# Performance work log

Hardware: AMD Instinct MI355X
Metric: run time of the kernel (lower is better)

The kernel has to match this reference:

```python
import jax, jax.numpy as jnp
import numpy as np

C_IN = 128      # in_channels == num_hiddens (required for residual add)
C_RES = 64      # num_residual_hiddens
D = 512         # representation_dim (in == out)


def _complete_conv1d(x, W, Wc, bc):
    """Faithful fused form of CompleteConv1d.forward for batch=1.

    x:  (1, C, D)   input
    W:  (C, D, D)   stacked per-channel Linear weights (W[c] maps D->D)
    Wc: (OC, C)     1x1 Conv1d weight (kernel dim squeezed)
    bc: (OC,)       1x1 Conv1d bias

    The autograd jacobian of the per-channel linear map is block diagonal:
      xy_grad[c, o, c', i] = W[c, o, i] * delta(c, c')
    so xy_grad_reduced[o, i] = sum_c W[c, o, i], node[i] = argmax_o of that,
    and the python double loop is a scatter-add:
      (y - y_neg)[0, f, n] = sum_{i : node[i]==n} W[f, n, i] * x[0, f, i]
    (y itself, including the Linear biases, cancels exactly).
    """
    d = W.shape[1]
    node = jnp.argmax(jnp.sum(W, axis=0), axis=0)          # (D,) argmax over o
    idx = jnp.arange(d)
    vals = W[:, node, idx] * x[0]                           # (C, D): W[f,node[i],i]*x[0,f,i]
    diff = jnp.zeros_like(x[0]).at[:, node].add(vals)       # scatter-add over repeated nodes
    out = jnp.einsum('oc,cd->od', Wc, diff) + bc[:, None]   # 1x1 conv == channel GEMM
    return out[None]                                        # (1, OC, D)


def setup_inputs() -> dict:
    key = jax.random.key(0)
    ks = jax.random.split(key, 7)
    s = lambda k, shape, scale: (jax.random.normal(k, shape, dtype=jnp.float32) * scale)
    return {
        'x':   s(ks[0], (1, C_IN, D), 1.0),
        'W1':  s(ks[1], (C_IN, D, D), D ** -0.5),
        'Wc1': s(ks[2], (C_RES, C_IN), C_IN ** -0.5),
        'bc1': s(ks[3], (C_RES,), 0.02),
        'W2':  s(ks[4], (C_RES, D, D), D ** -0.5),
        'Wc2': s(ks[5], (C_IN, C_RES), C_RES ** -0.5),
        'bc2': s(ks[6], (C_IN,), 0.02),
    }


def reference(x, W1, Wc1, bc1, W2, Wc2, bc2):
    # nn.ReLU(True) inside the Sequential mutates x in place, so the residual
    # add uses relu(x), not x.
    xr = jax.nn.relu(x)
    h1 = _complete_conv1d(xr, W1, Wc1, bc1)
    h2 = _complete_conv1d(jax.nn.relu(h1), W2, Wc2, bc2)
    return xr + h2
```

## Files before the change

kernel.cpp:

```cpp
#include <hip/hip_runtime.h>

#define C_IN  128
#define C_RES 64
#define D     512
#define DD    (D * D)

template <int C>
__device__ inline float4 colsum(const float4* __restrict__ Wp) {
    float4 acc = make_float4(0.f, 0.f, 0.f, 0.f);
#pragma unroll 16
    for (int c = 0; c < C; ++c) {
        float4 w = Wp[(size_t)c * (DD / 4)];
        acc.x += w.x; acc.y += w.y; acc.z += w.z; acc.w += w.w;
    }
    return acc;
}

__global__ void sum_zero_kernel(const float* __restrict__ W1,
                                const float* __restrict__ W2,
                                float* __restrict__ S1,
                                float* __restrict__ S2,
                                float* __restrict__ diff_zero) {
    int t = blockIdx.x * 256 + threadIdx.x;
    if (t < DD / 4) {
        ((float4*)S1)[t] = colsum<C_IN>((const float4*)W1 + t);
    } else {
        int t2 = t - DD / 4;
        ((float4*)S2)[t2] = colsum<C_RES>((const float4*)W2 + t2);
    }
    diff_zero[t] = 0.f;
}

__global__ void argmax_scatter_kernel(const float* __restrict__ S1,
                                      const float* __restrict__ S2,
                                      const float* __restrict__ W1,
                                      const float* __restrict__ W2,
                                      const float* __restrict__ x,
                                      float* __restrict__ diff1,
                                      float* __restrict__ w2v,
                                      int* __restrict__ node2) {
    __shared__ float lv[256];
    __shared__ int   li[256];
    __shared__ int   node_s[16];

    const int  tid = threadIdx.x;
    const bool st1 = blockIdx.x < 32;
    const int  i0  = (blockIdx.x & 31) * 16;
    const float* __restrict__ S = st1 ? S1 : S2;

    const int il = tid & 15;
    const int ol = tid >> 4;
    float best = -__builtin_inff();
    int   bidx = D;
#pragma unroll 4
    for (int k = 0; k < 32; ++k) {
        int o = ol + (k << 4);
        float v = S[o * D + i0 + il];
        if (v > best) { best = v; bidx = o; }
    }
    lv[tid] = best; li[tid] = bidx;
    __syncthreads();
    for (int s = 128; s >= 16; s >>= 1) {
        if (tid < s) {
            float v2 = lv[tid + s]; int i2 = li[tid + s];
            if (v2 > lv[tid] || (v2 == lv[tid] && i2 < li[tid])) {
                lv[tid] = v2; li[tid] = i2;
            }
        }
        __syncthreads();
    }
    if (tid < 16) {
        node_s[tid] = li[tid];
        if (!st1) node2[i0 + tid] = li[tid];
    }
    __syncthreads();

    if (st1) {
        for (int idx = tid; idx < C_IN * 16; idx += 256) {
            int ii = idx & 15;
            int c  = idx >> 4;
            int i  = i0 + ii;
            int n  = node_s[ii];
            float xv = fmaxf(x[c * D + i], 0.f);
            float w  = W1[(size_t)c * DD + (size_t)n * D + i];
            atomicAdd(&diff1[c * D + n], w * xv);
        }
    } else {
        for (int idx = tid; idx < C_RES * 16; idx += 256) {
            int ii = idx & 15;
            int c  = idx >> 4;
            int i  = i0 + ii;
            int n  = node_s[ii];
            w2v[c * D + i] = W2[(size_t)c * DD + (size_t)n * D + i];
        }
    }
}

__global__ void conv1_scatter2_kernel(const float* __restrict__ Wc1,
                                      const float* __restrict__ bc1,
                                      const float* __restrict__ diff1,
                                      const float* __restrict__ w2v,
                                      const int* __restrict__ node2,
                                      float* __restrict__ diff2) {
    __shared__ float wc[C_IN];
    const int c = blockIdx.x >> 1;
    const int i = ((blockIdx.x & 1) << 8) + threadIdx.x;
    if (threadIdx.x < C_IN) wc[threadIdx.x] = Wc1[c * C_IN + threadIdx.x];
    __syncthreads();

    float acc = bc1[c];
#pragma unroll 8
    for (int cc = 0; cc < C_IN; ++cc)
        acc += wc[cc] * diff1[cc * D + i];
    float x2 = fmaxf(acc, 0.f);
    int n = node2[i];
    atomicAdd(&diff2[c * D + n], w2v[c * D + i] * x2);
}

__global__ void final_kernel(const float* __restrict__ Wc2,
                             const float* __restrict__ bc2,
                             const float* __restrict__ diff2,
                             const float* __restrict__ x,
                             float* __restrict__ out) {
    __shared__ float wc[C_RES];
    const int o = blockIdx.x >> 1;
    const int d = ((blockIdx.x & 1) << 8) + threadIdx.x;
    if (threadIdx.x < C_RES) wc[threadIdx.x] = Wc2[o * C_RES + threadIdx.x];
    __syncthreads();

    float acc = bc2[o];
#pragma unroll 8
    for (int c = 0; c < C_RES; ++c)
        acc += wc[c] * diff2[c * D + d];
    out[o * D + d] = acc + fmaxf(x[o * D + d], 0.f);
}

extern "C" void kernel_launch(void* const* d_in, const int* in_sizes, int n_in,
                              void* d_out, int out_size, void* d_ws, size_t ws_size,
                              hipStream_t stream) {
    const float* x   = (const float*)d_in[0];
    const float* W1  = (const float*)d_in[1];
    const float* Wc1 = (const float*)d_in[2];
    const float* bc1 = (const float*)d_in[3];
    const float* W2  = (const float*)d_in[4];
    const float* Wc2 = (const float*)d_in[5];
    const float* bc2 = (const float*)d_in[6];
    float* out = (float*)d_out;

    float* ws    = (float*)d_ws;
    float* S1    = ws;
    float* S2    = S1 + DD;
    float* diff1 = S2 + DD;
    float* diff2 = diff1 + C_IN * D;
    float* w2v   = diff2 + C_RES * D;
    int*   node2 = (int*)(w2v + C_RES * D);

    sum_zero_kernel<<<384, 256, 0, stream>>>(W1, W2, S1, S2, diff1);
    argmax_scatter_kernel<<<64, 256, 0, stream>>>(S1, S2, W1, W2, x,
                                                  diff1, w2v, node2);
    conv1_scatter2_kernel<<<128, 256, 0, stream>>>(Wc1, bc1, diff1, w2v,
                                                   node2, diff2);
    final_kernel<<<256, 256, 0, stream>>>(Wc2, bc2, diff2, x, out);
}
```

Baseline: 256.5 us.

## Fuse all stages into one cooperative kernel with grid syncs and rebalanced colsum

Replaces the four separate kernel launches with a single cooperative kernel that separates its stages with grid.sync(). The W1 column sum is split into two 64-channel halves, so each of the 384 blocks does equal work (two 64-channel sums per thread) instead of some blocks summing 128 channels and others 64. The argmax/scatter stage now uses 128 blocks of 8 columns instead of 64 blocks of 16. This is meant to cut launch overhead and the load-imbalance tail, at the cost of grid-wide barriers and an extra partial-sum buffer that the argmax stage must read.

New measurement: 407.6 us. 58.9% more time.

```diff
diff --git a/kernel.cpp b/kernel.cpp
--- a/kernel.cpp
+++ b/kernel.cpp
@@ -1,138 +1,150 @@
 #include <hip/hip_runtime.h>
+#include <hip/hip_cooperative_groups.h>
+
+namespace cg = cooperative_groups;
 
 #define C_IN  128
 #define C_RES 64
 #define D     512
 #define DD    (D * D)
+#define NC4   (DD / 4)
 
-template <int C>
-__device__ inline float4 colsum(const float4* __restrict__ Wp) {
+__device__ __forceinline__ float4 colsum64(const float4* __restrict__ p) {
     float4 acc = make_float4(0.f, 0.f, 0.f, 0.f);
 #pragma unroll 16
-    for (int c = 0; c < C; ++c) {
-        float4 w = Wp[(size_t)c * (DD / 4)];
+    for (int c = 0; c < 64; ++c) {
+        float4 w = p[(size_t)c * NC4];
         acc.x += w.x; acc.y += w.y; acc.z += w.z; acc.w += w.w;
     }
     return acc;
 }
 
-__global__ void sum_zero_kernel(const float* __restrict__ W1,
-                                const float* __restrict__ W2,
-                                float* __restrict__ S1,
-                                float* __restrict__ S2,
-                                float* __restrict__ diff_zero) {
-    int t = blockIdx.x * 256 + threadIdx.x;
-    if (t < DD / 4) {
-        ((float4*)S1)[t] = colsum<C_IN>((const float4*)W1 + t);
-    } else {
-        int t2 = t - DD / 4;
-        ((float4*)S2)[t2] = colsum<C_RES>((const float4*)W2 + t2);
-    }
-    diff_zero[t] = 0.f;
-}
+__global__ void fused_kernel(const float* __restrict__ x,
+                             const float* __restrict__ W1,
+                             const float* __restrict__ Wc1,
+                             const float* __restrict__ bc1,
+                             const float* __restrict__ W2,
+                             const float* __restrict__ Wc2,
+                             const float* __restrict__ bc2,
+                             float* __restrict__ out,
+                             float* __restrict__ ws) {
+    cg::grid_group grid = cg::this_grid();
 
-__global__ void argmax_scatter_kernel(const float* __restrict__ S1,
-                                      const float* __restrict__ S2,
-                                      const float* __restrict__ W1,
-                                      const float* __restrict__ W2,
-                                      const float* __restrict__ x,
-                                      float* __restrict__ diff1,
-                                      float* __restrict__ w2v,
-                                      int* __restrict__ node2) {
+    float* S1lo  = ws;
+    float* S1hi  = S1lo + DD;
+    float* S2    = S1hi + DD;
+    float* diff1 = S2 + DD;
+    float* diff2 = diff1 + C_IN * D;
+    float* w2v   = diff2 + C_RES * D;
+    int*   node2 = (int*)(w2v + C_RES * D);
+
+    const int tid = threadIdx.x;
+    const int bid = blockIdx.x;
+    const int u   = bid * 256 + tid;
+
     __shared__ float lv[256];
     __shared__ int   li[256];
-    __shared__ int   node_s[16];
+    __shared__ int   node_s[8];
 
-    const int  tid = threadIdx.x;
-    const bool st1 = blockIdx.x < 32;
-    const int  i0  = (blockIdx.x & 31) * 16;
-    const float* __restrict__ S = st1 ? S1 : S2;
+    {
+        if (u < NC4) {
+            ((float4*)S1lo)[u] = colsum64((const float4*)W1 + u);
+        } else {
+            int t = u - NC4;
+            ((float4*)S1hi)[t] =
+                colsum64((const float4*)W1 + (size_t)64 * NC4 + t);
+        }
+        if (u < NC4 / 2) {
+            int t = u + NC4 / 2;
+            ((float4*)S1hi)[t] =
+                colsum64((const float4*)W1 + (size_t)64 * NC4 + t);
+        } else {
+            int t = u - NC4 / 2;
+            ((float4*)S2)[t] = colsum64((const float4*)W2 + t);
+        }
+        diff1[u] = 0.f;
+    }
+    grid.sync();
 
-    const int il = tid & 15;
-    const int ol = tid >> 4;
-    float best = -__builtin_inff();
-    int   bidx = D;
-#pragma unroll 4
-    for (int k = 0; k < 32; ++k) {
-        int o = ol + (k << 4);
-        float v = S[o * D + i0 + il];
-        if (v > best) { best = v; bidx = o; }
-    }
-    lv[tid] = best; li[tid] = bidx;
-    __syncthreads();
-    for (int s = 128; s >= 16; s >>= 1) {
-        if (tid < s) {
-            float v2 = lv[tid + s]; int i2 = li[tid + s];
-            if (v2 > lv[tid] || (v2 == lv[tid] && i2 < li[tid])) {
-                lv[tid] = v2; li[tid] = i2;
+    if (bid < 128) {
+        const bool st1 = bid < 64;
+        const int  i0  = (bid & 63) * 8;
+        const int  il  = tid & 7;
+        const int  ol  = tid >> 3;
+        float best = -__builtin_inff();
+        int   bidx = D;
+#pragma unroll
+        for (int k = 0; k < 16; ++k) {
+            int o = ol + (k << 5);
+            float v = st1 ? (S1lo[o * D + i0 + il] + S1hi[o * D + i0 + il])
+                          : S2[o * D + i0 + il];
+            if (v > best) { best = v; bidx = o; }
+        }
+        lv[tid] = best; li[tid] = bidx;
+        __syncthreads();
+        for (int s = 128; s >= 8; s >>= 1) {
+            if (tid < s) {
+                float v2 = lv[tid + s]; int i2 = li[tid + s];
+                if (v2 > lv[tid] || (v2 == lv[tid] && i2 < li[tid])) {
+                    lv[tid] = v2; li[tid] = i2;
+                }
+            }
+            __syncthreads();
+        }
+        if (tid < 8) {
+            node_s[tid] = li[tid];
+            if (!st1) node2[i0 + tid] = li[tid];
+        }
+        __syncthreads();
+
+        if (st1) {
+            for (int idx = tid; idx < C_IN * 8; idx += 256) {
+                int ii = idx & 7;
+                int c  = idx >> 3;
+                int i  = i0 + ii;
+                int n  = node_s[ii];
+                float xv = fmaxf(x[c * D + i], 0.f);
+                float w  = W1[(size_t)c * DD + (size_t)n * D + i];
+                atomicAdd(&diff1[c * D + n], w * xv);
+            }
+        } else {
+            for (int idx = tid; idx < C_RES * 8; idx += 256) {
+                int ii = idx & 7;
+                int c  = idx >> 3;
+                int i  = i0 + ii;
+                int n  = node_s[ii];
+                w2v[c * D + i] = W2[(size_t)c * DD + (size_t)n * D + i];
             }
         }
+    }
+    grid.sync();
+
+    if (bid < 128) {
+        const int c = bid >> 1;
+        const int i = ((bid & 1) << 8) + tid;
+        if (tid < C_IN) lv[tid] = Wc1[c * C_IN + tid];
         __syncthreads();
+        float acc = bc1[c];
+#pragma unroll 8
+        for (int cc = 0; cc < C_IN; ++cc)
+            acc += lv[cc] * diff1[cc * D + i];
+        float x2 = fmaxf(acc, 0.f);
+        int n = node2[i];
+        atomicAdd(&diff2[c * D + n], w2v[c * D + i] * x2);
     }
-    if (tid < 16) {
-        node_s[tid] = li[tid];
-        if (!st1) node2[i0 + tid] = li[tid];
+    grid.sync();
+
+    if (bid < 256) {
+        const int o = bid >> 1;
+        const int d = ((bid & 1) << 8) + tid;
+        if (tid < C_RES) lv[tid] = Wc2[o * C_RES + tid];
+        __syncthreads();
+        float acc = bc2[o];
+#pragma unroll 8
+        for (int c = 0; c < C_RES; ++c)
+            acc += lv[c] * diff2[c * D + d];
+        out[o * D + d] = acc + fmaxf(x[o * D + d], 0.f);
     }
-    __syncthreads();
-
-    if (st1) {
-        for (int idx = tid; idx < C_IN * 16; idx += 256) {
-            int ii = idx & 15;
-            int c  = idx >> 4;
-            int i  = i0 + ii;
-            int n  = node_s[ii];
-            float xv = fmaxf(x[c * D + i], 0.f);
-            float w  = W1[(size_t)c * DD + (size_t)n * D + i];
-            atomicAdd(&diff1[c * D + n], w * xv);
-        }
-    } else {
-        for (int idx = tid; idx < C_RES * 16; idx += 256) {
-            int ii = idx & 15;
-            int c  = idx >> 4;
-            int i  = i0 + ii;
-            int n  = node_s[ii];
-            w2v[c * D + i] = W2[(size_t)c * DD + (size_t)n * D + i];
-        }
-    }
-}
-
-__global__ void conv1_scatter2_kernel(const float* __restrict__ Wc1,
-                                      const float* __restrict__ bc1,
-                                      const float* __restrict__ diff1,
-                                      const float* __restrict__ w2v,
-                                      const int* __restrict__ node2,
-                                      float* __restrict__ diff2) {
-    __shared__ float wc[C_IN];
-    const int c = blockIdx.x >> 1;
-    const int i = ((blockIdx.x & 1) << 8) + threadIdx.x;
-    if (threadIdx.x < C_IN) wc[threadIdx.x] = Wc1[c * C_IN + threadIdx.x];
-    __syncthreads();
-
-    float acc = bc1[c];
-#pragma unroll 8
-    for (int cc = 0; cc < C_IN; ++cc)
-        acc += wc[cc] * diff1[cc * D + i];
-    float x2 = fmaxf(acc, 0.f);
-    int n = node2[i];
-    atomicAdd(&diff2[c * D + n], w2v[c * D + i] * x2);
-}
-
-__global__ void final_kernel(const float* __restrict__ Wc2,
-                             const float* __restrict__ bc2,
-                             const float* __restrict__ diff2,
-                             const float* __restrict__ x,
-                             float* __restrict__ out) {
-    __shared__ float wc[C_RES];
-    const int o = blockIdx.x >> 1;
-    const int d = ((blockIdx.x & 1) << 8) + threadIdx.x;
-    if (threadIdx.x < C_RES) wc[threadIdx.x] = Wc2[o * C_RES + threadIdx.x];
-    __syncthreads();
-
-    float acc = bc2[o];
-#pragma unroll 8
-    for (int c = 0; c < C_RES; ++c)
-        acc += wc[c] * diff2[c * D + d];
-    out[o * D + d] = acc + fmaxf(x[o * D + d], 0.f);
 }
 
 extern "C" void kernel_launch(void* const* d_in, const int* in_sizes, int n_in,
@@ -146,19 +158,10 @@
     const float* Wc2 = (const float*)d_in[5];
     const float* bc2 = (const float*)d_in[6];
     float* out = (float*)d_out;
+    float* ws  = (float*)d_ws;
 
-    float* ws    = (float*)d_ws;
-    float* S1    = ws;
-    float* S2    = S1 + DD;
-    float* diff1 = S2 + DD;
-    float* diff2 = diff1 + C_IN * D;
-    float* w2v   = diff2 + C_RES * D;
-    int*   node2 = (int*)(w2v + C_RES * D);
-
-    sum_zero_kernel<<<384, 256, 0, stream>>>(W1, W2, S1, S2, diff1);
-    argmax_scatter_kernel<<<64, 256, 0, stream>>>(S1, S2, W1, W2, x,
-                                                  diff1, w2v, node2);
-    conv1_scatter2_kernel<<<128, 256, 0, stream>>>(Wc1, bc1, diff1, w2v,
-                                                   node2, diff2);
-    final_kernel<<<256, 256, 0, stream>>>(Wc2, bc2, diff2, x, out);
+    void* args[] = {(void*)&x, (void*)&W1, (void*)&Wc1, (void*)&bc1,
+                    (void*)&W2, (void*)&Wc2, (void*)&bc2, (void*)&out, (void*)&ws};
+    hipLaunchCooperativeKernel((const void*)fused_kernel, dim3(384), dim3(256),
+                               args, 0, stream);
 }
```

## Split channel column-sum into partial planes and widen argmax grid

Applied to the files above, without the earlier changes.

The channel reduction of W1 and W2 is split into six 32-channel partial-sum planes, so the first kernel launches 1536 blocks instead of 384 and gives the memory-bound pass over roughly 200 MB of weights more parallelism. The argmax kernel finishes the reduction by adding four or two partial planes per element. It now handles 4 columns per block across 256 blocks instead of 16 columns across 64. This costs extra workspace and extra partial-sum traffic in exchange for better bandwidth use and occupancy.

Result: slower. 267.9 us (+4.4%).

```diff
diff --git a/kernel.cpp b/kernel.cpp
--- a/kernel.cpp
+++ b/kernel.cpp
@@ -4,35 +4,29 @@
 #define C_RES 64
 #define D     512
 #define DD    (D * D)
-
-template <int C>
-__device__ inline float4 colsum(const float4* __restrict__ Wp) {
-    float4 acc = make_float4(0.f, 0.f, 0.f, 0.f);
-#pragma unroll 16
-    for (int c = 0; c < C; ++c) {
-        float4 w = Wp[(size_t)c * (DD / 4)];
-        acc.x += w.x; acc.y += w.y; acc.z += w.z; acc.w += w.w;
-    }
-    return acc;
-}
+#define NC4   (DD / 4)
 
 __global__ void sum_zero_kernel(const float* __restrict__ W1,
                                 const float* __restrict__ W2,
-                                float* __restrict__ S1,
-                                float* __restrict__ S2,
+                                float* __restrict__ Sp,
                                 float* __restrict__ diff_zero) {
     int t = blockIdx.x * 256 + threadIdx.x;
-    if (t < DD / 4) {
-        ((float4*)S1)[t] = colsum<C_IN>((const float4*)W1 + t);
-    } else {
-        int t2 = t - DD / 4;
-        ((float4*)S2)[t2] = colsum<C_RES>((const float4*)W2 + t2);
+    int plane = t >> 16;
+    int chunk = t & 0xFFFF;
+    const float4* p = (plane < 4)
+        ? (const float4*)W1 + (size_t)plane * 32 * NC4 + chunk
+        : (const float4*)W2 + (size_t)(plane - 4) * 32 * NC4 + chunk;
+    float4 acc = make_float4(0.f, 0.f, 0.f, 0.f);
+#pragma unroll 16
+    for (int c = 0; c < 32; ++c) {
+        float4 w = p[(size_t)c * NC4];
+        acc.x += w.x; acc.y += w.y; acc.z += w.z; acc.w += w.w;
     }
-    diff_zero[t] = 0.f;
+    ((float4*)Sp)[t] = acc;
+    if (t < (C_IN + C_RES) * D) diff_zero[t] = 0.f;
 }
 
-__global__ void argmax_scatter_kernel(const float* __restrict__ S1,
-                                      const float* __restrict__ S2,
+__global__ void argmax_scatter_kernel(const float* __restrict__ Sp,
                                       const float* __restrict__ W1,
                                       const float* __restrict__ W2,
                                       const float* __restrict__ x,
@@ -41,26 +35,32 @@
                                       int* __restrict__ node2) {
     __shared__ float lv[256];
     __shared__ int   li[256];
-    __shared__ int   node_s[16];
+    __shared__ int   node_s[4];
 
     const int  tid = threadIdx.x;
-    const bool st1 = blockIdx.x < 32;
-    const int  i0  = (blockIdx.x & 31) * 16;
-    const float* __restrict__ S = st1 ? S1 : S2;
+    const bool st1 = blockIdx.x < 128;
+    const int  i0  = (blockIdx.x & 127) * 4;
+    const int  il  = tid & 3;
+    const int  ol  = tid >> 2;
+    const float* __restrict__ S1p = Sp;
+    const float* __restrict__ S2p = Sp + (size_t)4 * DD;
 
-    const int il = tid & 15;
-    const int ol = tid >> 4;
     float best = -__builtin_inff();
     int   bidx = D;
-#pragma unroll 4
-    for (int k = 0; k < 32; ++k) {
-        int o = ol + (k << 4);
-        float v = S[o * D + i0 + il];
+#pragma unroll
+    for (int k = 0; k < 8; ++k) {
+        int o   = ol + (k << 6);
+        int off = o * D + i0 + il;
+        float v;
+        if (st1)
+            v = S1p[off] + S1p[DD + off] + S1p[2 * DD + off] + S1p[3 * DD + off];
+        else
+            v = S2p[off] + S2p[DD + off];
         if (v > best) { best = v; bidx = o; }
     }
     lv[tid] = best; li[tid] = bidx;
     __syncthreads();
-    for (int s = 128; s >= 16; s >>= 1) {
+    for (int s = 128; s >= 4; s >>= 1) {
         if (tid < s) {
             float v2 = lv[tid + s]; int i2 = li[tid + s];
             if (v2 > lv[tid] || (v2 == lv[tid] && i2 < li[tid])) {
@@ -69,16 +69,16 @@
         }
         __syncthreads();
     }
-    if (tid < 16) {
+    if (tid < 4) {
         node_s[tid] = li[tid];
         if (!st1) node2[i0 + tid] = li[tid];
     }
     __syncthreads();
 
     if (st1) {
-        for (int idx = tid; idx < C_IN * 16; idx += 256) {
-            int ii = idx & 15;
-            int c  = idx >> 4;
+        for (int idx = tid; idx < C_IN * 4; idx += 256) {
+            int ii = idx & 3;
+            int c  = idx >> 2;
             int i  = i0 + ii;
             int n  = node_s[ii];
             float xv = fmaxf(x[c * D + i], 0.f);
@@ -86,9 +86,9 @@
             atomicAdd(&diff1[c * D + n], w * xv);
         }
     } else {
-        for (int idx = tid; idx < C_RES * 16; idx += 256) {
-            int ii = idx & 15;
-            int c  = idx >> 4;
+        for (int idx = tid; idx < C_RES * 4; idx += 256) {
+            int ii = idx & 3;
+            int c  = idx >> 2;
             int i  = i0 + ii;
             int n  = node_s[ii];
             w2v[c * D + i] = W2[(size_t)c * DD + (size_t)n * D + i];
@@ -148,16 +148,15 @@
     float* out = (float*)d_out;
 
     float* ws    = (float*)d_ws;
-    float* S1    = ws;
-    float* S2    = S1 + DD;
-    float* diff1 = S2 + DD;
+    float* Sp    = ws;
+    float* diff1 = Sp + (size_t)6 * DD;
     float* diff2 = diff1 + C_IN * D;
     float* w2v   = diff2 + C_RES * D;
     int*   node2 = (int*)(w2v + C_RES * D);
 
-    sum_zero_kernel<<<384, 256, 0, stream>>>(W1, W2, S1, S2, diff1);
-    argmax_scatter_kernel<<<64, 256, 0, stream>>>(S1, S2, W1, W2, x,
-                                                  diff1, w2v, node2);
+    sum_zero_kernel<<<1536, 256, 0, stream>>>(W1, W2, Sp, diff1);
+    argmax_scatter_kernel<<<256, 256, 0, stream>>>(Sp, W1, W2, x,
+                                                   diff1, w2v, node2);
     conv1_scatter2_kernel<<<128, 256, 0, stream>>>(Wc1, bc1, diff1, w2v,
                                                    node2, diff2);
     final_kernel<<<256, 256, 0, stream>>>(Wc2, bc2, diff2, x, out);
```

## Balance column-sum work by splitting W1 sum and fuse tail conv stages

Applied to the files above, without the earlier changes.

The column-sum kernel now gives every thread two 64-channel column sums, with W1 split into low and high halves that the argmax kernel adds back together, so the W1 and W2 threads carry equal load. The output is initialized with relu(x)+bc2 during the first kernel. The two 1x1-conv kernels are merged into one tail kernel that computes h1 for 8 positions per block and then applies Wc2 before scattering, using linearity so the diff2 buffer and a launch go away. This trades extra atomics into out and a duplicated Wc1 load per block for removing the load imbalance and one kernel launch.

Measured after the change: 290.9 us. +13.4%, slower.

```diff
diff --git a/kernel.cpp b/kernel.cpp
--- a/kernel.cpp
+++ b/kernel.cpp
@@ -4,41 +4,58 @@
 #define C_RES 64
 #define D     512
 #define DD    (D * D)
+#define NC4   (DD / 4)
 
-template <int C>
-__device__ inline float4 colsum(const float4* __restrict__ Wp) {
+__device__ __forceinline__ float4 colsum64(const float4* __restrict__ p) {
     float4 acc = make_float4(0.f, 0.f, 0.f, 0.f);
 #pragma unroll 16
-    for (int c = 0; c < C; ++c) {
-        float4 w = Wp[(size_t)c * (DD / 4)];
+    for (int c = 0; c < 64; ++c) {
+        float4 w = p[(size_t)c * NC4];
         acc.x += w.x; acc.y += w.y; acc.z += w.z; acc.w += w.w;
     }
     return acc;
 }
 
-__global__ void sum_zero_kernel(const float* __restrict__ W1,
-                                const float* __restrict__ W2,
-                                float* __restrict__ S1,
-                                float* __restrict__ S2,
-                                float* __restrict__ diff_zero) {
-    int t = blockIdx.x * 256 + threadIdx.x;
-    if (t < DD / 4) {
-        ((float4*)S1)[t] = colsum<C_IN>((const float4*)W1 + t);
+__global__ __launch_bounds__(256)
+void sum_init_kernel(const float* __restrict__ W1,
+                     const float* __restrict__ W2,
+                     const float* __restrict__ x,
+                     const float* __restrict__ bc2,
+                     float* __restrict__ S1lo,
+                     float* __restrict__ S1hi,
+                     float* __restrict__ S2,
+                     float* __restrict__ diff1,
+                     float* __restrict__ out) {
+    const int u = blockIdx.x * 256 + threadIdx.x;
+    if (u < NC4) {
+        ((float4*)S1lo)[u] = colsum64((const float4*)W1 + u);
     } else {
-        int t2 = t - DD / 4;
-        ((float4*)S2)[t2] = colsum<C_RES>((const float4*)W2 + t2);
+        int t = u - NC4;
+        ((float4*)S1hi)[t] = colsum64((const float4*)W1 + (size_t)64 * NC4 + t);
     }
-    diff_zero[t] = 0.f;
+    if (u < NC4 / 2) {
+        int t = u + NC4 / 2;
+        ((float4*)S1hi)[t] = colsum64((const float4*)W1 + (size_t)64 * NC4 + t);
+    } else {
+        int t = u - NC4 / 2;
+        ((float4*)S2)[t] = colsum64((const float4*)W2 + t);
+    }
+    if (u < C_IN * D) {
+        diff1[u] = 0.f;
+        out[u] = fmaxf(x[u], 0.f) + bc2[u >> 9];
+    }
 }
 
-__global__ void argmax_scatter_kernel(const float* __restrict__ S1,
-                                      const float* __restrict__ S2,
-                                      const float* __restrict__ W1,
-                                      const float* __restrict__ W2,
-                                      const float* __restrict__ x,
-                                      float* __restrict__ diff1,
-                                      float* __restrict__ w2v,
-                                      int* __restrict__ node2) {
+__global__ __launch_bounds__(256)
+void argmax_scatter_kernel(const float* __restrict__ S1lo,
+                           const float* __restrict__ S1hi,
+                           const float* __restrict__ S2,
+                           const float* __restrict__ W1,
+                           const float* __restrict__ W2,
+                           const float* __restrict__ x,
+                           float* __restrict__ diff1,
+                           float* __restrict__ w2v,
+                           int* __restrict__ node2) {
     __shared__ float lv[256];
     __shared__ int   li[256];
     __shared__ int   node_s[16];
@@ -46,16 +63,16 @@
     const int  tid = threadIdx.x;
     const bool st1 = blockIdx.x < 32;
     const int  i0  = (blockIdx.x & 31) * 16;
-    const float* __restrict__ S = st1 ? S1 : S2;
+    const int  il  = tid & 15;
+    const int  ol  = tid >> 4;
 
-    const int il = tid & 15;
-    const int ol = tid >> 4;
     float best = -__builtin_inff();
     int   bidx = D;
 #pragma unroll 4
     for (int k = 0; k < 32; ++k) {
-        int o = ol + (k << 4);
-        float v = S[o * D + i0 + il];
+        int o   = ol + (k << 4);
+        int off = o * D + i0 + il;
+        float v = st1 ? (S1lo[off] + S1hi[off]) : S2[off];
         if (v > best) { best = v; bidx = o; }
     }
     lv[tid] = best; li[tid] = bidx;
@@ -96,43 +113,62 @@
     }
 }
 
-__global__ void conv1_scatter2_kernel(const float* __restrict__ Wc1,
-                                      const float* __restrict__ bc1,
-                                      const float* __restrict__ diff1,
-                                      const float* __restrict__ w2v,
-                                      const int* __restrict__ node2,
-                                      float* __restrict__ diff2) {
-    __shared__ float wc[C_IN];
-    const int c = blockIdx.x >> 1;
-    const int i = ((blockIdx.x & 1) << 8) + threadIdx.x;
-    if (threadIdx.x < C_IN) wc[threadIdx.x] = Wc1[c * C_IN + threadIdx.x];
+__global__ __launch_bounds__(256)
+void tail_kernel(const float* __restrict__ Wc1,
+                 const float* __restrict__ bc1,
+                 const float* __restrict__ diff1,
+                 const float* __restrict__ w2v,
+                 const int* __restrict__ node2,
+                 const float* __restrict__ Wc2,
+                 float* __restrict__ out) {
+    __shared__ float wc1s[C_RES][C_IN + 1];
+    __shared__ float d1s[C_IN][8];
+    __shared__ float ts[C_RES][9];
+    __shared__ int   nds[8];
+
+    const int tid = threadIdx.x;
+    const int i0  = blockIdx.x * 8;
+
+    for (int idx = tid; idx < C_RES * C_IN; idx += 256)
+        wc1s[idx >> 7][idx & 127] = Wc1[idx];
+    for (int idx = tid; idx < C_IN * 8; idx += 256)
+        d1s[idx >> 3][idx & 7] = diff1[(idx >> 3) * D + i0 + (idx & 7)];
+    if (tid < 8) nds[tid] = node2[i0 + tid];
     __syncthreads();
 
-    float acc = bc1[c];
+    {
+        const int c = tid & 63;
+        const int j = tid >> 6;
+        float a0 = bc1[c];
+        float a1 = a0;
 #pragma unroll 8
-    for (int cc = 0; cc < C_IN; ++cc)
-        acc += wc[cc] * diff1[cc * D + i];
-    float x2 = fmaxf(acc, 0.f);
-    int n = node2[i];
-    atomicAdd(&diff2[c * D + n], w2v[c * D + i] * x2);
-}
-
-__global__ void final_kernel(const float* __restrict__ Wc2,
-                             const float* __restrict__ bc2,
-                             const float* __restrict__ diff2,
-                             const float* __restrict__ x,
-                             float* __restrict__ out) {
-    __shared__ float wc[C_RES];
-    const int o = blockIdx.x >> 1;
-    const int d = ((blockIdx.x & 1) << 8) + threadIdx.x;
-    if (threadIdx.x < C_RES) wc[threadIdx.x] = Wc2[o * C_RES + threadIdx.x];
+        for (int cc = 0; cc < C_IN; ++cc) {
+            float w = wc1s[c][cc];
+            a0 += w * d1s[cc][2 * j];
+            a1 += w * d1s[cc][2 * j + 1];
+        }
+        ts[c][2 * j]     = w2v[c * D + i0 + 2 * j]     * fmaxf(a0, 0.f);
+        ts[c][2 * j + 1] = w2v[c * D + i0 + 2 * j + 1] * fmaxf(a1, 0.f);
+    }
     __syncthreads();
 
-    float acc = bc2[o];
+    {
+        const int o = tid >> 1;
+        const int h = tid & 1;
+        float z0 = 0.f, z1 = 0.f, z2 = 0.f, z3 = 0.f;
 #pragma unroll 8
-    for (int c = 0; c < C_RES; ++c)
-        acc += wc[c] * diff2[c * D + d];
-    out[o * D + d] = acc + fmaxf(x[o * D + d], 0.f);
+        for (int c = 0; c < C_RES; ++c) {
+            float w = Wc2[o * C_RES + c];
+            z0 += w * ts[c][4 * h];
+            z1 += w * ts[c][4 * h + 1];
+            z2 += w * ts[c][4 * h + 2];
+            z3 += w * ts[c][4 * h + 3];
+        }
+        atomicAdd(&out[o * D + nds[4 * h]],     z0);
+        atomicAdd(&out[o * D + nds[4 * h + 1]], z1);
+        atomicAdd(&out[o * D + nds[4 * h + 2]], z2);
+        atomicAdd(&out[o * D + nds[4 * h + 3]], z3);
+    }
 }
 
 extern "C" void kernel_launch(void* const* d_in, const int* in_sizes, int n_in,
@@ -148,17 +184,16 @@
     float* out = (float*)d_out;
 
     float* ws    = (float*)d_ws;
-    float* S1    = ws;
-    float* S2    = S1 + DD;
+    float* S1lo  = ws;
+    float* S1hi  = S1lo + DD;
+    float* S2    = S1hi + DD;
     float* diff1 = S2 + DD;
-    float* diff2 = diff1 + C_IN * D;
-    float* w2v   = diff2 + C_RES * D;
+    float* w2v   = diff1 + C_IN * D;
     int*   node2 = (int*)(w2v + C_RES * D);
 
-    sum_zero_kernel<<<384, 256, 0, stream>>>(W1, W2, S1, S2, diff1);
-    argmax_scatter_kernel<<<64, 256, 0, stream>>>(S1, S2, W1, W2, x,
+    sum_init_kernel<<<384, 256, 0, stream>>>(W1, W2, x, bc2,
+                                             S1lo, S1hi, S2, diff1, out);
+    argmax_scatter_kernel<<<64, 256, 0, stream>>>(S1lo, S1hi, S2, W1, W2, x,
                                                   diff1, w2v, node2);
-    conv1_scatter2_kernel<<<128, 256, 0, stream>>>(Wc1, bc1, diff1, w2v,
-                                                   node2, diff2);
-    final_kernel<<<256, 256, 0, stream>>>(Wc2, bc2, diff2, x, out);
+    tail_kernel<<<64, 256, 0, stream>>>(Wc1, bc1, diff1, w2v, node2, Wc2, out);
 }
```
